# Kernel tuning notes

Hardware: AMD Instinct MI355X
Metric: run time of the kernel (lower is better)

The kernel has to match this reference:

```python
import jax, jax.numpy as jnp
import numpy as np

B, L, DIM, N_STATE, K_CONV = 2, 2048, 1024, 16, 4


def setup_inputs() -> dict:
    key = jax.random.key(0)
    ks = jax.random.split(key, 6)
    sc = lambda k, shape, s: jax.random.normal(k, shape, jnp.float32) * s
    return {
        "x": jax.random.normal(ks[0], (B, L, DIM), jnp.float32),
        "in_proj_w": sc(ks[1], (2 * DIM, DIM), 0.02),
        "conv_w": sc(ks[2], (DIM, 1, K_CONV), 0.1),
        "conv_b": jnp.zeros((DIM,), jnp.float32),
        "x_proj_w": sc(ks[3], (2 * N_STATE + DIM, DIM), 0.02),
        "D_param": jnp.ones((DIM,), jnp.float32),
        "out_proj_w": sc(ks[4], (DIM, DIM), 0.02),
    }


def reference(x, in_proj_w, conv_w, conv_b, x_proj_w, D_param, out_proj_w):
    b, l, d = x.shape
    n = (x_proj_w.shape[0] - d) // 2
    k = conv_w.shape[-1]
    # A buffer: -[1..n] broadcast over channels -> [d, n]
    A = -(jnp.arange(1, n + 1, dtype=x.dtype)[None, :] * jnp.ones((d, 1), x.dtype))

    xz = x @ in_proj_w.T                       # [b, l, 2d]
    x_c, z = xz[..., :d], xz[..., d:]

    # depthwise causal conv (torch pads both sides k-1 then truncates to l == left-pad k-1)
    xc = jnp.transpose(x_c, (0, 2, 1))          # [b, d, l]
    xc = jax.lax.conv_general_dilated(
        xc, conv_w, window_strides=(1,), padding=[(k - 1, 0)],
        dimension_numbers=("NCH", "OIH", "NCH"), feature_group_count=d)
    xc = xc + conv_b[None, :, None]
    xc = jax.nn.silu(jnp.transpose(xc, (0, 2, 1)))  # [b, l, d]

    x_dbl = xc @ x_proj_w.T                    # [b, l, 2n + d]
    B_ssm = x_dbl[..., :n]                     # [b, l, n]
    C_ssm = x_dbl[..., n:2 * n]                # [b, l, n]
    dt = jax.nn.softplus(x_dbl[..., 2 * n:])   # [b, l, d]

    dA = jnp.exp(dt[..., None] * A[None, None])            # [b, l, d, n]
    dBx = (dt[..., None] * B_ssm[:, :, None, :]) * xc[..., None]  # dB * x, [b, l, d, n]

    def step(h, inputs):
        dA_t, dBx_t, C_t = inputs              # [b,d,n], [b,d,n], [b,n]
        h = h * dA_t + dBx_t
        y_t = jnp.einsum("bdn,bn->bd", h, C_t)
        return h, y_t

    h0 = jnp.zeros((b, d, n), x.dtype)
    _, ys = jax.lax.scan(
        step, h0,
        (jnp.moveaxis(dA, 1, 0), jnp.moveaxis(dBx, 1, 0), jnp.moveaxis(C_ssm, 1, 0)))
    y = jnp.moveaxis(ys, 0, 1) + D_param * xc  # [b, l, d]
    y = y * jax.nn.silu(z)
    return y @ out_proj_w.T
```

## Files before the change

kernel.cpp:

```cpp
#include <hip/hip_runtime.h>
#include <cmath>

#define BB   2
#define LL   2048
#define DIMD 1024
#define NS   16
#define KC   4
#define ML   (BB*LL)
#define XZ_N (2*DIMD)
#define XD_N (2*NS + DIMD)
#define LC   16
#define NC   (LL/LC)

typedef __attribute__((ext_vector_type(8))) short bf16x8;
typedef __attribute__((ext_vector_type(4))) float f32x4;

__device__ __forceinline__ unsigned short f2bf(float f) {
    union { float f; unsigned u; } v; v.f = f;
    unsigned r = v.u + 0x7FFF + ((v.u >> 16) & 1);
    return (unsigned short)(r >> 16);
}
__device__ __forceinline__ float bf2f(unsigned short u) {
    union { unsigned u; float f; } v; v.u = (unsigned)u << 16;
    return v.f;
}
__device__ __forceinline__ float silu_f(float a) {
    return a / (1.f + __expf(-a));
}
__device__ __forceinline__ void dt_decay(float raw, float& dt, float& e) {
    const float t = __expf(fminf(raw, 80.f));
    e  = 1.f / (1.f + t);
    dt = (raw > 15.f) ? raw : -__logf(e);
}

__global__ __launch_bounds__(256) void cvt_all(
    const float* __restrict__ s0, unsigned short* __restrict__ d0, int n0,
    const float* __restrict__ s1, unsigned short* __restrict__ d1, int n1,
    const float* __restrict__ s2, unsigned short* __restrict__ d2, int n2,
    const float* __restrict__ s3, unsigned short* __restrict__ d3, int n3)
{
    int i = blockIdx.x * blockDim.x + threadIdx.x;
    const float* src; unsigned short* dst;
    if (i < n0)                { src = s0; dst = d0; }
    else if ((i -= n0) < n1)   { src = s1; dst = d1; }
    else if ((i -= n1) < n2)   { src = s2; dst = d2; }
    else if ((i -= n2) < n3)   { src = s3; dst = d3; }
    else return;
    float4 f = ((const float4*)src)[i];
    ushort4 o;
    o.x = f2bf(f.x); o.y = f2bf(f.y); o.z = f2bf(f.z); o.w = f2bf(f.w);
    ((ushort4*)dst)[i] = o;
}

__global__ __launch_bounds__(256) void gemm_mfma_bt(
    const unsigned short* __restrict__ A,
    const unsigned short* __restrict__ Bw,
    float* __restrict__ C,
    unsigned short* __restrict__ zb,
    int M, int N, int K, int nsplit)
{
    __shared__ short As[128 * 64];
    __shared__ short Bs[128 * 64];

    const int nwg  = gridDim.x * gridDim.y;
    int wgid = blockIdx.y * gridDim.x + blockIdx.x;
    const int cpx = nwg >> 3;
    wgid = (wgid & 7) * cpx + (wgid >> 3);
    const int bx = wgid % gridDim.x;
    const int by = wgid / gridDim.x;

    const int tid  = threadIdx.x;
    const int lane = tid & 63;
    const int wave = tid >> 6;
    const int bm = by * 128;
    const int bn = bx * 128;
    const int wm = (wave >> 1) * 64;
    const int wn = (wave & 1) * 64;
    const int l15  = lane & 15;
    const int quad = lane >> 4;

    f32x4 acc[4][4];
    #pragma unroll
    for (int i = 0; i < 4; ++i)
        #pragma unroll
        for (int j = 0; j < 4; ++j)
            acc[i][j] = (f32x4){0.f, 0.f, 0.f, 0.f};

    for (int k0 = 0; k0 < K; k0 += 64) {
        __syncthreads();
        #pragma unroll
        for (int q = 0; q < 4; ++q) {
            const int ci = q * 256 + tid;
            const int r  = ci >> 3;
            const int cc = (ci & 7) ^ (r & 7);
            short* ldsA = As + (size_t)(q * 256 + (tid & ~63)) * 8;
            const unsigned short* ga = A + (size_t)(bm + r) * K + k0 + cc * 8;
            __builtin_amdgcn_global_load_lds(
                (const __attribute__((address_space(1))) void*)ga,
                (__attribute__((address_space(3))) void*)ldsA, 16, 0, 0);
        }
        #pragma unroll
        for (int q = 0; q < 4; ++q) {
            const int ci = q * 256 + tid;
            const int r  = ci >> 3;
            const int cc = (ci & 7) ^ (r & 7);
            short* ldsB = Bs + (size_t)(q * 256 + (tid & ~63)) * 8;
            int rb = bn + r; if (rb > N - 1) rb = N - 1;
            const unsigned short* gb = Bw + (size_t)rb * K + k0 + cc * 8;
            __builtin_amdgcn_global_load_lds(
                (const __attribute__((address_space(1))) void*)gb,
                (__attribute__((address_space(3))) void*)ldsB, 16, 0, 0);
        }
        __syncthreads();

        #pragma unroll
        for (int kh = 0; kh < 2; ++kh) {
            bf16x8 af[4], bfr[4];
            #pragma unroll
            for (int i = 0; i < 4; ++i) {
                const int row = wm + i * 16 + l15;
                const int pc  = (kh * 4 + quad) ^ (row & 7);
                af[i] = *(const bf16x8*)(As + row * 64 + pc * 8);
            }
            #pragma unroll
            for (int j = 0; j < 4; ++j) {
                const int row = wn + j * 16 + l15;
                const int pc  = (kh * 4 + quad) ^ (row & 7);
                bfr[j] = *(const bf16x8*)(Bs + row * 64 + pc * 8);
            }
            #pragma unroll
            for (int i = 0; i < 4; ++i)
                #pragma unroll
                for (int j = 0; j < 4; ++j)
                    acc[i][j] = __builtin_amdgcn_mfma_f32_16x16x32_bf16(
                        af[i], bfr[j], acc[i][j], 0, 0, 0);
        }
    }

    #pragma unroll
    for (int i = 0; i < 4; ++i) {
        const int rbase = bm + wm + i * 16 + quad * 4;
        #pragma unroll
        for (int j = 0; j < 4; ++j) {
            const int col = bn + wn + j * 16 + l15;
            if (col < nsplit) {
                #pragma unroll
                for (int r = 0; r < 4; ++r)
                    C[(size_t)(rbase + r) * nsplit + col] = acc[i][j][r];
            } else if (col < N) {
                const int zc = col - nsplit;
                #pragma unroll
                for (int r = 0; r < 4; ++r)
                    zb[(size_t)(rbase + r) * DIMD + zc] = f2bf(silu_f(acc[i][j][r]));
            }
        }
    }
}

__global__ __launch_bounds__(256) void conv_silu(const float* __restrict__ xcraw,
                                                 const float* __restrict__ w,
                                                 const float* __restrict__ bias,
                                                 float* __restrict__ xc,
                                                 unsigned short* __restrict__ xcb)
{
    const int i4 = blockIdx.x * blockDim.x + threadIdx.x;
    if (i4 >= ML * DIMD / 4) return;
    const int dq = i4 & (DIMD / 4 - 1);
    const int bl = i4 >> 8;
    const int l  = bl & (LL - 1);

    const float4 wq0 = ((const float4*)w)[dq * 4 + 0];
    const float4 wq1 = ((const float4*)w)[dq * 4 + 1];
    const float4 wq2 = ((const float4*)w)[dq * 4 + 2];
    const float4 wq3 = ((const float4*)w)[dq * 4 + 3];
    const float4 bv  = ((const float4*)bias)[dq];

    const float* p = xcraw + (size_t)bl * DIMD + dq * 4;
    const float4 z4 = make_float4(0.f, 0.f, 0.f, 0.f);
    const float4 x0 = (l >= 3) ? *(const float4*)(p - 3 * DIMD) : z4;
    const float4 x1 = (l >= 2) ? *(const float4*)(p - 2 * DIMD) : z4;
    const float4 x2 = (l >= 1) ? *(const float4*)(p - 1 * DIMD) : z4;
    const float4 x3 = *(const float4*)p;

    float4 a;
    a.x = bv.x + wq0.x*x0.x + wq0.y*x1.x + wq0.z*x2.x + wq0.w*x3.x;
    a.y = bv.y + wq1.x*x0.y + wq1.y*x1.y + wq1.z*x2.y + wq1.w*x3.y;
    a.z = bv.z + wq2.x*x0.z + wq2.y*x1.z + wq2.z*x2.z + wq2.w*x3.z;
    a.w = bv.w + wq3.x*x0.w + wq3.y*x1.w + wq3.z*x2.w + wq3.w*x3.w;

    float4 v;
    v.x = silu_f(a.x); v.y = silu_f(a.y); v.z = silu_f(a.z); v.w = silu_f(a.w);

    ((float4*)xc)[i4] = v;
    ushort4 o;
    o.x = f2bf(v.x); o.y = f2bf(v.y); o.z = f2bf(v.z); o.w = f2bf(v.w);
    ((ushort4*)xcb)[i4] = o;
}

__global__ __launch_bounds__(256) void scan_part1(const float* __restrict__ xdbl,
                                                  const float* __restrict__ xc,
                                                  float* __restrict__ hfin,
                                                  float* __restrict__ Ssum)
{
    __shared__ float Bsh[LC][NS];

    const int tid = threadIdx.x;
    const int idx = blockIdx.x * 256 + tid;
    const int d   = idx & (DIMD - 1);
    const int bc  = idx >> 10;
    const int c   = bc & (NC - 1);
    const int b   = bc >> 7;
    const int l0  = c * LC;

    const float* xdbl_p = xdbl + ((size_t)b * LL + l0) * XD_N;
    const float* xc_p   = xc   + ((size_t)b * LL + l0) * DIMD + d;

    if (tid < LC * NS / 4) {
        const int l = tid >> 2, q = tid & 3;
        ((float4*)&Bsh[l][0])[q] = ((const float4*)(xdbl_p + (size_t)l * XD_N))[q];
    }
    __syncthreads();

    float raw[LC], xcv[LC];
    #pragma unroll
    for (int i = 0; i < LC; ++i) raw[i] = xdbl_p[(size_t)i * XD_N + 2 * NS + d];
    #pragma unroll
    for (int i = 0; i < LC; ++i) xcv[i] = xc_p[(size_t)i * DIMD];

    float e[LC], dx[LC];
    float S = 0.f;
    #pragma unroll
    for (int i = 0; i < LC; ++i) {
        float dt, ev;
        dt_decay(raw[i], dt, ev);
        S += dt;
        e[i]  = ev;
        dx[i] = dt * xcv[i];
    }

    float h[NS];
    #pragma unroll
    for (int n = 0; n < NS; ++n) h[n] = 0.f;

    #pragma unroll
    for (int i = 0; i < LC; ++i) {
        const float4* BC = (const float4*)&Bsh[i][0];
        const float4 B0 = BC[0], B1 = BC[1], B2 = BC[2], B3 = BC[3];
        const float ev = e[i], dxv = dx[i];
        const float e2 = ev * ev, e4 = e2 * e2;
        float p0 = ev, p1 = e2, p2 = e2 * ev, p3 = e4;
        h[0]  = fmaf(h[0],  p0, dxv * B0.x);
        h[1]  = fmaf(h[1],  p1, dxv * B0.y);
        h[2]  = fmaf(h[2],  p2, dxv * B0.z);
        h[3]  = fmaf(h[3],  p3, dxv * B0.w);
        p0 *= e4; p1 *= e4; p2 *= e4; p3 *= e4;
        h[4]  = fmaf(h[4],  p0, dxv * B1.x);
        h[5]  = fmaf(h[5],  p1, dxv * B1.y);
        h[6]  = fmaf(h[6],  p2, dxv * B1.z);
        h[7]  = fmaf(h[7],  p3, dxv * B1.w);
        p0 *= e4; p1 *= e4; p2 *= e4; p3 *= e4;
        h[8]  = fmaf(h[8],  p0, dxv * B2.x);
        h[9]  = fmaf(h[9],  p1, dxv * B2.y);
        h[10] = fmaf(h[10], p2, dxv * B2.z);
        h[11] = fmaf(h[11], p3, dxv * B2.w);
        p0 *= e4; p1 *= e4; p2 *= e4; p3 *= e4;
        h[12] = fmaf(h[12], p0, dxv * B3.x);
        h[13] = fmaf(h[13], p1, dxv * B3.y);
        h[14] = fmaf(h[14], p2, dxv * B3.z);
        h[15] = fmaf(h[15], p3, dxv * B3.w);
    }

    float4* hf = (float4*)(hfin + (size_t)idx * NS);
    #pragma unroll
    for (int n = 0; n < 4; ++n) hf[n] = ((float4*)h)[n];
    Ssum[idx] = S;
}

__global__ __launch_bounds__(256) void scan_combine(float* __restrict__ hfin,
                                                    const float* __restrict__ Ssum)
{
    const int idx = blockIdx.x * blockDim.x + threadIdx.x;
    const int n = idx & (NS - 1);
    const int d = (idx >> 4) & (DIMD - 1);
    const int b = idx >> 14;
    const float np1 = (float)(n + 1);

    float hc = 0.f;
    for (int c0 = 0; c0 < NC; c0 += 8) {
        float Sb[8], hb[8], eb[8];
        #pragma unroll
        for (int j = 0; j < 8; ++j) {
            const size_t base = ((size_t)(b * NC + c0 + j) * DIMD + d);
            Sb[j] = Ssum[base];
            hb[j] = hfin[base * NS + n];
        }
        #pragma unroll
        for (int j = 0; j < 8; ++j) eb[j] = __expf(-Sb[j] * np1);
        #pragma unroll
        for (int j = 0; j < 8; ++j) {
            const size_t o = ((size_t)(b * NC + c0 + j) * DIMD + d) * NS + n;
            hfin[o] = hc;
            hc = fmaf(hc, eb[j], hb[j]);
        }
    }
}

__global__ __launch_bounds__(256) void scan_part2(const float* __restrict__ xdbl,
                                                  const float* __restrict__ xc,
                                                  const unsigned short* __restrict__ zb,
                                                  const float* __restrict__ hfin,
                                                  const float* __restrict__ Dp,
                                                  unsigned short* __restrict__ yout)
{
    __shared__ float BCs[LC][2 * NS];

    const int tid = threadIdx.x;
    const int idx = blockIdx.x * 256 + tid;
    const int d   = idx & (DIMD - 1);
    const int bc  = idx >> 10;
    const int c   = bc & (NC - 1);
    const int b   = bc >> 7;
    const int l0  = c * LC;

    const float* xdbl_p = xdbl + ((size_t)b * LL + l0) * XD_N;
    const float* xc_p   = xc   + ((size_t)b * LL + l0) * DIMD + d;
    const unsigned short* zb_p = zb + ((size_t)b * LL + l0) * DIMD + d;
    unsigned short* y_p = yout + ((size_t)b * LL + l0) * DIMD + d;

    if (tid < LC * 2 * NS / 4) {
        const int l = tid >> 3, q = tid & 7;
        ((float4*)&BCs[l][0])[q] = ((const float4*)(xdbl_p + (size_t)l * XD_N))[q];
    }
    __syncthreads();

    float raw[LC], xcv[LC], zg[LC];
    #pragma unroll
    for (int i = 0; i < LC; ++i) raw[i] = xdbl_p[(size_t)i * XD_N + 2 * NS + d];
    #pragma unroll
    for (int i = 0; i < LC; ++i) xcv[i] = xc_p[(size_t)i * DIMD];
    #pragma unroll
    for (int i = 0; i < LC; ++i) zg[i] = bf2f(zb_p[(size_t)i * DIMD]);

    float e[LC], dx[LC];
    #pragma unroll
    for (int i = 0; i < LC; ++i) {
        float dt, ev;
        dt_decay(raw[i], dt, ev);
        e[i]  = ev;
        dx[i] = dt * xcv[i];
    }

    const float Dv = Dp[d];
    float h[NS];
    {
        const float4* hf = (const float4*)(hfin + (size_t)idx * NS);
        #pragma unroll
        for (int n = 0; n < 4; ++n) ((float4*)h)[n] = hf[n];
    }

    #pragma unroll
    for (int i = 0; i < LC; ++i) {
        const float4* BC = (const float4*)&BCs[i][0];
        const float4 B0 = BC[0], B1 = BC[1], B2 = BC[2], B3 = BC[3];
        const float4 C0 = BC[4], C1 = BC[5], C2 = BC[6], C3 = BC[7];
        const float ev = e[i], dxv = dx[i];
        const float e2 = ev * ev, e4 = e2 * e2;
        float p0 = ev, p1 = e2, p2 = e2 * ev, p3 = e4;
        float y0, y1, y2, y3;
        h[0]  = fmaf(h[0],  p0, dxv * B0.x); y0 = h[0]  * C0.x;
        h[1]  = fmaf(h[1],  p1, dxv * B0.y); y1 = h[1]  * C0.y;
        h[2]  = fmaf(h[2],  p2, dxv * B0.z); y2 = h[2]  * C0.z;
        h[3]  = fmaf(h[3],  p3, dxv * B0.w); y3 = h[3]  * C0.w;
        p0 *= e4; p1 *= e4; p2 *= e4; p3 *= e4;
        h[4]  = fmaf(h[4],  p0, dxv * B1.x); y0 = fmaf(h[4],  C1.x, y0);
        h[5]  = fmaf(h[5],  p1, dxv * B1.y); y1 = fmaf(h[5],  C1.y, y1);
        h[6]  = fmaf(h[6],  p2, dxv * B1.z); y2 = fmaf(h[6],  C1.z, y2);
        h[7]  = fmaf(h[7],  p3, dxv * B1.w); y3 = fmaf(h[7],  C1.w, y3);
        p0 *= e4; p1 *= e4; p2 *= e4; p3 *= e4;
        h[8]  = fmaf(h[8],  p0, dxv * B2.x); y0 = fmaf(h[8],  C2.x, y0);
        h[9]  = fmaf(h[9],  p1, dxv * B2.y); y1 = fmaf(h[9],  C2.y, y1);
        h[10] = fmaf(h[10], p2, dxv * B2.z); y2 = fmaf(h[10], C2.z, y2);
        h[11] = fmaf(h[11], p3, dxv * B2.w); y3 = fmaf(h[11], C2.w, y3);
        p0 *= e4; p1 *= e4; p2 *= e4; p3 *= e4;
        h[12] = fmaf(h[12], p0, dxv * B3.x); y0 = fmaf(h[12], C3.x, y0);
        h[13] = fmaf(h[13], p1, dxv * B3.y); y1 = fmaf(h[13], C3.y, y1);
        h[14] = fmaf(h[14], p2, dxv * B3.z); y2 = fmaf(h[14], C3.z, y2);
        h[15] = fmaf(h[15], p3, dxv * B3.w); y3 = fmaf(h[15], C3.w, y3);

        const float y  = (y0 + y1) + (y2 + y3);
        const float yv = fmaf(Dv, xcv[i], y);
        y_p[(size_t)i * DIMD] = f2bf(yv * zg[i]);
    }
}

extern "C" void kernel_launch(void* const* d_in, const int* in_sizes, int n_in,
                              void* d_out, int out_size, void* d_ws, size_t ws_size,
                              hipStream_t stream)
{
    const float* x          = (const float*)d_in[0];
    const float* in_proj_w  = (const float*)d_in[1];
    const float* conv_w     = (const float*)d_in[2];
    const float* conv_b     = (const float*)d_in[3];
    const float* x_proj_w   = (const float*)d_in[4];
    const float* D_param    = (const float*)d_in[5];
    const float* out_proj_w = (const float*)d_in[6];
    float* out = (float*)d_out;

    float* xcraw = (float*)d_ws;
    float* xc    = xcraw + (size_t)ML * DIMD;
    float* xdbl  = xc    + (size_t)ML * DIMD;
    unsigned short* zb  = (unsigned short*)(xdbl + (size_t)ML * XD_N);
    unsigned short* xb  = zb  + (size_t)ML * DIMD;
    unsigned short* xcb = xb  + (size_t)ML * DIMD;
    unsigned short* wb1 = xcb + (size_t)ML * DIMD;
    unsigned short* wb2 = wb1 + (size_t)XZ_N * DIMD;
    unsigned short* wb3 = wb2 + (size_t)XD_N * DIMD;
    float* hfin = (float*)(wb3 + (size_t)DIMD * DIMD);
    float* Ssum = hfin + (size_t)BB * NC * DIMD * NS;
    unsigned short* yb  = xb;

    const int n0 = ML * DIMD / 4, n1 = XZ_N * DIMD / 4,
              n2 = XD_N * DIMD / 4, n3 = DIMD * DIMD / 4;
    const int ncvt = n0 + n1 + n2 + n3;

    cvt_all<<<(ncvt + 255) / 256, 256, 0, stream>>>(
        x, xb, n0, in_proj_w, wb1, n1, x_proj_w, wb2, n2, out_proj_w, wb3, n3);

    gemm_mfma_bt<<<dim3(XZ_N / 128, ML / 128), 256, 0, stream>>>(
        xb, wb1, xcraw, zb, ML, XZ_N, DIMD, DIMD);

    conv_silu<<<(ML * DIMD / 4) / 256, 256, 0, stream>>>(
        xcraw, conv_w, conv_b, xc, xcb);

    gemm_mfma_bt<<<dim3((XD_N + 127) / 128, ML / 128), 256, 0, stream>>>(
        xcb, wb2, xdbl, nullptr, ML, XD_N, DIMD, XD_N);

    scan_part1<<<(BB * NC * DIMD) / 256, 256, 0, stream>>>(xdbl, xc, hfin, Ssum);
    scan_combine<<<(BB * DIMD * NS) / 256, 256, 0, stream>>>(hfin, Ssum);
    scan_part2<<<(BB * NC * DIMD) / 256, 256, 0, stream>>>(xdbl, xc, zb, hfin,
                                                           D_param, yb);

    gemm_mfma_bt<<<dim3(DIMD / 128, ML / 128), 256, 0, stream>>>(
        yb, wb3, out, nullptr, ML, DIMD, DIMD, DIMD);
}
```

Measured before the change: 220.4 us.

## Restructure GEMM to single-wave 64x64 tiles with triple-buffered async LDS loads

Changes the bf16 MFMA GEMM from 256-thread 128x128 tiles to one-wave 64x64 tiles. Tiles are staged through a three-deep ring of LDS buffers using global_load_lds and explicit vmcnt waits instead of __syncthreads. Prefetching two k-steps ahead is meant to hide global load latency, and the smaller tiles produce more workgroups. In exchange each output tile reuses less data, so global and L2 traffic rise. The pipeline also depends on the exact count of outstanding loads being right.

```diff
diff --git a/kernel.cpp b/kernel.cpp
--- a/kernel.cpp
+++ b/kernel.cpp
@@ -52,15 +52,15 @@
     ((ushort4*)dst)[i] = o;
 }
 
-__global__ __launch_bounds__(256) void gemm_mfma_bt(
+__global__ __launch_bounds__(64) void gemm_mfma_bt(
     const unsigned short* __restrict__ A,
     const unsigned short* __restrict__ Bw,
     float* __restrict__ C,
     unsigned short* __restrict__ zb,
     int M, int N, int K, int nsplit)
 {
-    __shared__ short As[128 * 64];
-    __shared__ short Bs[128 * 64];
+    __shared__ short As[3 * 64 * 64];
+    __shared__ short Bs[3 * 64 * 64];
 
     const int nwg  = gridDim.x * gridDim.y;
     int wgid = blockIdx.y * gridDim.x + blockIdx.x;
@@ -69,13 +69,9 @@
     const int bx = wgid % gridDim.x;
     const int by = wgid / gridDim.x;
 
-    const int tid  = threadIdx.x;
-    const int lane = tid & 63;
-    const int wave = tid >> 6;
-    const int bm = by * 128;
-    const int bn = bx * 128;
-    const int wm = (wave >> 1) * 64;
-    const int wn = (wave & 1) * 64;
+    const int lane = threadIdx.x;
+    const int bm = by * 64;
+    const int bn = bx * 64;
     const int l15  = lane & 15;
     const int quad = lane >> 4;
 
@@ -86,47 +82,68 @@
         for (int j = 0; j < 4; ++j)
             acc[i][j] = (f32x4){0.f, 0.f, 0.f, 0.f};
 
-    for (int k0 = 0; k0 < K; k0 += 64) {
-        __syncthreads();
-        #pragma unroll
-        for (int q = 0; q < 4; ++q) {
-            const int ci = q * 256 + tid;
+    const int NK = K >> 6;
+
+    auto stage = [&](int s, int kt) {
+        const int k0 = kt * 64;
+        #pragma unroll
+        for (int q = 0; q < 8; ++q) {
+            const int ci = q * 64 + lane;
             const int r  = ci >> 3;
             const int cc = (ci & 7) ^ (r & 7);
-            short* ldsA = As + (size_t)(q * 256 + (tid & ~63)) * 8;
             const unsigned short* ga = A + (size_t)(bm + r) * K + k0 + cc * 8;
             __builtin_amdgcn_global_load_lds(
                 (const __attribute__((address_space(1))) void*)ga,
-                (__attribute__((address_space(3))) void*)ldsA, 16, 0, 0);
-        }
-        #pragma unroll
-        for (int q = 0; q < 4; ++q) {
-            const int ci = q * 256 + tid;
+                (__attribute__((address_space(3))) void*)(As + s * 4096 + q * 512),
+                16, 0, 0);
+        }
+        #pragma unroll
+        for (int q = 0; q < 8; ++q) {
+            const int ci = q * 64 + lane;
             const int r  = ci >> 3;
             const int cc = (ci & 7) ^ (r & 7);
-            short* ldsB = Bs + (size_t)(q * 256 + (tid & ~63)) * 8;
             int rb = bn + r; if (rb > N - 1) rb = N - 1;
             const unsigned short* gb = Bw + (size_t)rb * K + k0 + cc * 8;
             __builtin_amdgcn_global_load_lds(
                 (const __attribute__((address_space(1))) void*)gb,
-                (__attribute__((address_space(3))) void*)ldsB, 16, 0, 0);
-        }
-        __syncthreads();
-
+                (__attribute__((address_space(3))) void*)(Bs + s * 4096 + q * 512),
+                16, 0, 0);
+        }
+    };
+
+    stage(0, 0);
+    stage(1, 1);
+
+    int cur = 0;
+    for (int t = 0; t < NK; ++t) {
+        if (t < NK - 1) {
+            asm volatile("s_waitcnt vmcnt(16)" ::: "memory");
+        } else {
+            asm volatile("s_waitcnt vmcnt(0)" ::: "memory");
+        }
+        __builtin_amdgcn_sched_barrier(0);
+
+        if (t + 2 < NK) {
+            int s2 = cur + 2; if (s2 >= 3) s2 -= 3;
+            stage(s2, t + 2);
+        }
+
+        const short* Ab = As + cur * 4096;
+        const short* Bb = Bs + cur * 4096;
         #pragma unroll
         for (int kh = 0; kh < 2; ++kh) {
             bf16x8 af[4], bfr[4];
             #pragma unroll
             for (int i = 0; i < 4; ++i) {
-                const int row = wm + i * 16 + l15;
+                const int row = i * 16 + l15;
                 const int pc  = (kh * 4 + quad) ^ (row & 7);
-                af[i] = *(const bf16x8*)(As + row * 64 + pc * 8);
+                af[i] = *(const bf16x8*)(Ab + row * 64 + pc * 8);
             }
             #pragma unroll
             for (int j = 0; j < 4; ++j) {
-                const int row = wn + j * 16 + l15;
+                const int row = j * 16 + l15;
                 const int pc  = (kh * 4 + quad) ^ (row & 7);
-                bfr[j] = *(const bf16x8*)(Bs + row * 64 + pc * 8);
+                bfr[j] = *(const bf16x8*)(Bb + row * 64 + pc * 8);
             }
             #pragma unroll
             for (int i = 0; i < 4; ++i)
@@ -135,14 +152,15 @@
                     acc[i][j] = __builtin_amdgcn_mfma_f32_16x16x32_bf16(
                         af[i], bfr[j], acc[i][j], 0, 0, 0);
         }
+        cur = cur + 1; if (cur >= 3) cur = 0;
     }
 
     #pragma unroll
     for (int i = 0; i < 4; ++i) {
-        const int rbase = bm + wm + i * 16 + quad * 4;
+        const int rbase = bm + i * 16 + quad * 4;
         #pragma unroll
         for (int j = 0; j < 4; ++j) {
-            const int col = bn + wn + j * 16 + l15;
+            const int col = bn + j * 16 + l15;
             if (col < nsplit) {
                 #pragma unroll
                 for (int r = 0; r < 4; ++r)
@@ -426,13 +444,13 @@
     cvt_all<<<(ncvt + 255) / 256, 256, 0, stream>>>(
         x, xb, n0, in_proj_w, wb1, n1, x_proj_w, wb2, n2, out_proj_w, wb3, n3);
 
-    gemm_mfma_bt<<<dim3(XZ_N / 128, ML / 128), 256, 0, stream>>>(
+    gemm_mfma_bt<<<dim3(XZ_N / 64, ML / 64), 64, 0, stream>>>(
         xb, wb1, xcraw, zb, ML, XZ_N, DIMD, DIMD);
 
     conv_silu<<<(ML * DIMD / 4) / 256, 256, 0, stream>>>(
         xcraw, conv_w, conv_b, xc, xcb);
 
-    gemm_mfma_bt<<<dim3((XD_N + 127) / 128, ML / 128), 256, 0, stream>>>(
+    gemm_mfma_bt<<<dim3((XD_N + 63) / 64, ML / 64), 64, 0, stream>>>(
         xcb, wb2, xdbl, nullptr, ML, XD_N, DIMD, XD_N);
 
     scan_part1<<<(BB * NC * DIMD) / 256, 256, 0, stream>>>(xdbl, xc, hfin, Ssum);
@@ -440,6 +458,6 @@
     scan_part2<<<(BB * NC * DIMD) / 256, 256, 0, stream>>>(xdbl, xc, zb, hfin,
                                                            D_param, yb);
 
-    gemm_mfma_bt<<<dim3(DIMD / 128, ML / 128), 256, 0, stream>>>(
+    gemm_mfma_bt<<<dim3(DIMD / 64, ML / 64), 64, 0, stream>>>(
         yb, wb3, out, nullptr, ML, DIMD, DIMD, DIMD);
 }
```

Measured after the change: 258.3 us. 1.17x slower.
